# Performance work log

Measured on AMD Instinct MI355X. Metric: run time of the kernel, lower is better.

The kernel has to match this reference:

```python
import jax, jax.numpy as jnp
import numpy as np

K_DEPTH = 3
JAC_A = 1.0  # alpha (Jacobi a)
JAC_B = 1.0  # beta  (Jacobi b)


def jacobi_filter(sig, gammas):
    """Polynomial graph filter g(sigma) = sum_k gamma_k * P_k^{(a,b)}(sigma),
    Jacobi recurrence applied elementwise (Sigma is diagonal spectrum), domain [-1,1],
    fixed inner scalings (fixI=True => alphas=1)."""
    a, b = JAC_A, JAC_B
    xs = [jnp.ones_like(sig)]
    # L = 1
    coef1 = (a - b) / 2.0
    coef2 = (a + b + 2.0) / 2.0
    xs.append(coef1 * xs[0] + coef2 * sig * xs[0])
    for L in range(2, K_DEPTH + 1):
        cl = 2.0 * L * (L + a + b) * (2 * L - 2 + a + b)
        c1 = (2 * L + a + b - 1) * (2 * L + a + b) * (2 * L + a + b - 2)
        c2 = (2 * L + a + b - 1) * (a * a - b * b)
        c3 = 2.0 * (L - 1 + a) * (L - 1 + b) * (2 * L + a + b)
        xs.append((c1 / cl) * sig * xs[-1] - (c2 / cl) * xs[-1] - (c3 / cl) * xs[-2])
    basis = jnp.stack(xs, axis=0)  # [K+1, B, H, L, d]
    return jnp.einsum('k,kbhld->bhld', gammas, basis)


def setup_inputs() -> dict:
    key = jax.random.key(0)
    ks = jax.random.split(key, 7)
    B, L, Ha, Hs, d = 4, 2048, 4, 4, 64
    mk = lambda k, H: jax.random.normal(k, (B, L, H, d), dtype=jnp.float32)
    return {
        'U': mk(ks[0], Ha),
        'Sigma': mk(ks[1], Ha),
        'V': mk(ks[2], Ha),
        'values': mk(ks[3], Ha),
        'queries_softmax': mk(ks[4], Hs),
        'keys_softmax': mk(ks[5], Hs),
        'values_softmax': mk(ks[6], Hs),
        'gammas': jnp.ones((K_DEPTH + 1,), dtype=jnp.float32),
    }


def reference(U, Sigma, V, values, queries_softmax, keys_softmax, values_softmax, gammas):
    d_k = U.shape[-1]
    # ---- AGF (SVD) heads ----
    Uh = jax.nn.softmax(jnp.transpose(U, (0, 2, 1, 3)), axis=-1)        # [B,H,L,d]
    Vt = jax.nn.softmax(jnp.transpose(V, (0, 2, 3, 1)), axis=-1)        # [B,H,d,L]
    vals = jnp.transpose(values, (0, 2, 1, 3))                           # [B,H,L,d]
    sig = jax.nn.sigmoid(jnp.transpose(Sigma, (0, 2, 1, 3)))             # [B,H,L,d]
    gf = jacobi_filter(sig, gammas)                                       # [B,H,L,d]
    kv = jnp.einsum('bhdl,bhle->bhde', Vt, vals)                          # [B,H,d,d]
    out_agf = jnp.einsum('bhld,bhde->bhle', Uh * gf, kv)                  # [B,H,L,d]
    out_agf = jnp.transpose(out_agf, (0, 2, 1, 3))                        # [B,L,H,d]
    # ---- orthogonality loss ----
    eye = jnp.eye(d_k, dtype=Uh.dtype)
    sym_u = jnp.einsum('bhld,bhle->bhde', Uh, Uh) - eye
    sym_v = jnp.einsum('bhdl,bhel->bhde', Vt, Vt) - eye
    ortho_loss = jnp.mean(jnp.abs(sym_u), axis=(1, 2, 3)) + jnp.mean(jnp.abs(sym_v), axis=(1, 2, 3))
    # ---- softmax (flash) heads ----
    q = jnp.transpose(queries_softmax, (0, 2, 1, 3))
    k = jnp.transpose(keys_softmax, (0, 2, 1, 3))
    v = jnp.transpose(values_softmax, (0, 2, 1, 3))
    scores = jnp.einsum('bhld,bhsd->bhls', q, k) / jnp.sqrt(jnp.asarray(d_k, q.dtype))
    attn = jax.nn.softmax(scores, axis=-1)
    out_sm = jnp.einsum('bhls,bhsd->bhld', attn, v)
    out_sm = jnp.transpose(out_sm, (0, 2, 1, 3))                          # [B,L,H,d]
    out = jnp.concatenate([out_agf, out_sm], axis=2)                      # [B,L,2H,d]
    return out, ortho_loss
```

## Files before the change

kernel.cpp:

```cpp
#include <hip/hip_runtime.h>
#include <hip/hip_bf16.h>

#define BB 4
#define SEQ 2048
#define NH 4
#define D 64
#define NPAIR 16
#define HOUT 8
#define LOSS_BASE ((size_t)BB * SEQ * HOUT * D)

#define OFF_PART 0
#define N_PART   (8 * 16 * 3 * 4096)
#define OFF_SPART (OFF_PART + N_PART)
#define N_SPART  (16 * 32 * 64)
#define OFF_LPART (OFF_SPART + N_SPART)
#define N_LPART  (2 * 16 * 4 * 2048)
#define OFF_OPART (OFF_LPART + N_LPART)
#define N_OPART  (2 * 16 * 2048 * 64)
#define OFF_US   (OFF_OPART + N_OPART)
#define USZ ((size_t)16 * 2048 * 64)

typedef __attribute__((ext_vector_type(8))) short bf16x8;
typedef __attribute__((ext_vector_type(4))) float f32x4;
typedef __attribute__((ext_vector_type(8))) unsigned short us8;
typedef __attribute__((ext_vector_type(4))) unsigned short us4;

__device__ __forceinline__ unsigned short f2bf(float x) {
    union { float f; unsigned u; } v; v.f = x;
    unsigned r = v.u + 0x7fffu + ((v.u >> 16) & 1u);
    return (unsigned short)(r >> 16);
}
__device__ __forceinline__ float bf2f(unsigned short u) {
    union { unsigned u; float f; } v; v.u = ((unsigned)u) << 16; return v.f;
}
__device__ __forceinline__ void load16(const float* p, float* v) {
    const float4* q = (const float4*)p;
    float4 a = q[0], b = q[1], c = q[2], d = q[3];
    v[0]=a.x; v[1]=a.y; v[2]=a.z; v[3]=a.w;
    v[4]=b.x; v[5]=b.y; v[6]=b.z; v[7]=b.w;
    v[8]=c.x; v[9]=c.y; v[10]=c.z; v[11]=c.w;
    v[12]=d.x; v[13]=d.y; v[14]=d.z; v[15]=d.w;
}
__device__ __forceinline__ void wr_bf16x16(unsigned short* dst, const float* v) {
    us8 w0, w1;
#pragma unroll
    for (int i = 0; i < 8; i++) { w0[i] = f2bf(v[i]); w1[i] = f2bf(v[8 + i]); }
    *(us8*)dst = w0; *(us8*)(dst + 8) = w1;
}

__global__ __launch_bounds__(256) void prep(const float* __restrict__ U, const float* __restrict__ Vagf,
                                            const float* __restrict__ vals, const float* __restrict__ Ksm,
                                            const float* __restrict__ Vsm,
                                            float* __restrict__ ws, unsigned short* __restrict__ usb,
                                            float* __restrict__ out) {
    int lt = blockIdx.x, p = blockIdx.y;
    int b = p >> 2, h = p & 3;
    int tid = threadIdx.x;
    int r = tid >> 2;
    int c4 = tid & 3;
    int c0 = c4 * 16;
    __shared__ float T[64][68];
    unsigned short* Khi   = usb;
    unsigned short* VbfT  = usb + USZ;
    unsigned short* UhT   = usb + 2 * USZ;
    unsigned short* EhiT  = usb + 3 * USZ;
    unsigned short* EloT  = usb + 4 * USZ;
    unsigned short* valsT = usb + 5 * USZ;
    float* Spart = ws + OFF_SPART;

    const size_t gbase = ((size_t)(b * SEQ + lt * 64 + r) * NH + h) * D + c0;
    const size_t tbase = ((size_t)p * 64 + r) * 2048 + lt * 64 + c0;
    float v[16], e[16];

    load16(U + gbase, v);
    float mx = v[0];
#pragma unroll
    for (int k = 1; k < 16; k++) mx = fmaxf(mx, v[k]);
    mx = fmaxf(mx, __shfl_xor(mx, 1));
    mx = fmaxf(mx, __shfl_xor(mx, 2));
    float sm = 0.0f;
#pragma unroll
    for (int k = 0; k < 16; k++) { v[k] = __expf(v[k] - mx); sm += v[k]; }
    sm += __shfl_xor(sm, 1);
    sm += __shfl_xor(sm, 2);
    float inv = 1.0f / sm;
#pragma unroll
    for (int k = 0; k < 16; k++) T[r][c0 + k] = v[k] * inv;
    __syncthreads();
#pragma unroll
    for (int k = 0; k < 16; k++) e[k] = T[c0 + k][r];
    wr_bf16x16(UhT + tbase, e);
    __syncthreads();

    load16(Vagf + gbase, v);
#pragma unroll
    for (int k = 0; k < 16; k++) T[r][c0 + k] = __expf(v[k]);
    __syncthreads();
    float ssum = 0.0f;
#pragma unroll
    for (int k = 0; k < 16; k++) { e[k] = T[c0 + k][r]; ssum += e[k]; }
    ssum += __shfl_xor(ssum, 1);
    ssum += __shfl_xor(ssum, 2);
    if (c4 == 0) Spart[(p * 32 + lt) * 64 + r] = ssum;
    {
        us8 h0, h1, l0, l1;
#pragma unroll
        for (int i = 0; i < 8; i++) {
            unsigned short hh = f2bf(e[i]);
            h0[i] = hh; l0[i] = f2bf(e[i] - bf2f(hh));
            unsigned short h2 = f2bf(e[8 + i]);
            h1[i] = h2; l1[i] = f2bf(e[8 + i] - bf2f(h2));
        }
        *(us8*)(EhiT + tbase) = h0; *(us8*)(EhiT + tbase + 8) = h1;
        *(us8*)(EloT + tbase) = l0; *(us8*)(EloT + tbase + 8) = l1;
    }
    __syncthreads();

    load16(vals + gbase, v);
#pragma unroll
    for (int k = 0; k < 16; k++) T[r][c0 + k] = v[k];
    __syncthreads();
#pragma unroll
    for (int k = 0; k < 16; k++) e[k] = T[c0 + k][r];
    wr_bf16x16(valsT + tbase, e);
    __syncthreads();

    load16(Vsm + gbase, v);
#pragma unroll
    for (int k = 0; k < 16; k++) T[r][c0 + k] = v[k];
    __syncthreads();
#pragma unroll
    for (int k = 0; k < 16; k++) e[k] = T[c0 + k][r];
    wr_bf16x16(VbfT + tbase, e);

    load16(Ksm + gbase, v);
    wr_bf16x16(Khi + ((size_t)(p * SEQ + lt * 64 + r)) * 64 + c0, v);

    if (lt == 0 && p == 0 && tid < BB) out[LOSS_BASE + tid] = 0.0f;
}

#define PSTR 72
#define FIXM 10.0f

__global__ __launch_bounds__(256, 3) void mid(const unsigned short* __restrict__ usb,
                                              const float* __restrict__ Q,
                                              float* __restrict__ part,
                                              float* __restrict__ Opart, float* __restrict__ lpart) {
    __shared__ __align__(16) unsigned char smem[20480];
    const int bid = blockIdx.x;
    const int tid = threadIdx.x;
    const int w = tid >> 6, lane = tid & 63, lm = lane & 15, quad = lane >> 4;

    if (bid < 1024) {
        int qt = bid & 31, p = (bid >> 5) & 15, half = bid >> 9;
        int b = p >> 2, h = p & 3;
        const unsigned short* Khi  = usb;
        const unsigned short* VbfT = usb + USZ;
        unsigned short* Ph = (unsigned short*)smem;

        bf16x8 qhi[4][2], qlo[4][2];
#pragma unroll
        for (int nq = 0; nq < 4; nq++) {
            const float* qp = Q + ((size_t)(b * SEQ + qt * 64 + nq * 16 + lm) * NH + h) * D + quad * 8;
#pragma unroll
            for (int ks = 0; ks < 2; ks++) {
                float4 a0 = *(const float4*)(qp + ks * 32);
                float4 a1 = *(const float4*)(qp + ks * 32 + 4);
                float qq[8] = {a0.x, a0.y, a0.z, a0.w, a1.x, a1.y, a1.z, a1.w};
#pragma unroll
                for (int j = 0; j < 8; j++) {
                    float xs = qq[j] * 0.125f;
                    unsigned short hi = f2bf(xs);
                    qhi[nq][ks][j] = (short)hi;
                    qlo[nq][ks][j] = (short)f2bf(xs - bf2f(hi));
                }
            }
        }

        float rsum[4] = {0.f, 0.f, 0.f, 0.f};
        f32x4 o[4];
#pragma unroll
        for (int t = 0; t < 4; t++) o[t] = (f32x4){0.f, 0.f, 0.f, 0.f};

        const size_t kbase = ((size_t)p * SEQ + (size_t)half * 1024 + w * 16 + lm) * 64 + quad * 8;
        const size_t vbase = ((size_t)p * 64 + w * 16 + lm) * 2048 + (size_t)half * 1024 + quad * 8;
        bf16x8 kf[2], vf[2], kf2[2], vf2[2];
#pragma unroll
        for (int ks = 0; ks < 2; ks++) {
            kf[ks] = *(const bf16x8*)(Khi + kbase + ks * 32);
            vf[ks] = *(const bf16x8*)(VbfT + vbase + ks * 32);
        }

        for (int it = 0; it < 16; ++it) {
            f32x4 s[4];
#pragma unroll
            for (int t = 0; t < 4; t++) s[t] = (f32x4){0.f, 0.f, 0.f, 0.f};
#pragma unroll
            for (int ks = 0; ks < 2; ks++)
#pragma unroll
                for (int nq = 0; nq < 4; nq++) {
                    s[nq] = __builtin_amdgcn_mfma_f32_16x16x32_bf16(kf[ks], qhi[nq][ks], s[nq], 0, 0, 0);
                    s[nq] = __builtin_amdgcn_mfma_f32_16x16x32_bf16(kf[ks], qlo[nq][ks], s[nq], 0, 0, 0);
                }
            if (it < 15) {
#pragma unroll
                for (int ks = 0; ks < 2; ks++) {
                    kf2[ks] = *(const bf16x8*)(Khi + kbase + (it + 1) * 64ull * 64 + ks * 32);
                    vf2[ks] = *(const bf16x8*)(VbfT + vbase + (it + 1) * 64 + ks * 32);
                }
            }
#pragma unroll
            for (int nq = 0; nq < 4; nq++) {
                us4 pk;
#pragma unroll
                for (int r = 0; r < 4; r++) {
                    float e = __expf(s[nq][r] - FIXM);
                    rsum[nq] += e;
                    pk[r] = f2bf(e);
                }
                *(us4*)&Ph[(nq * 16 + lm) * PSTR + w * 16 + quad * 4] = pk;
            }
            __syncthreads();

#pragma unroll
            for (int ks = 0; ks < 2; ks++)
#pragma unroll
                for (int nq = 0; nq < 4; nq++) {
                    bf16x8 pf = *(const bf16x8*)&Ph[(nq * 16 + lm) * PSTR + ks * 32 + quad * 8];
                    o[nq] = __builtin_amdgcn_mfma_f32_16x16x32_bf16(vf[ks], pf, o[nq], 0, 0, 0);
                }
            __syncthreads();
#pragma unroll
            for (int ks = 0; ks < 2; ks++) { kf[ks] = kf2[ks]; vf[ks] = vf2[ks]; }
        }

#pragma unroll
        for (int nq = 0; nq < 4; nq++) {
            float rs = rsum[nq];
            rs += __shfl_xor(rs, 16);
            rs += __shfl_xor(rs, 32);
            int row = qt * 64 + nq * 16 + lm;
            *(f32x4*)(Opart + ((size_t)(half * 16 + p) * SEQ + row) * 64 + w * 16 + quad * 4) = o[nq];
            if (quad == 0)
                lpart[((size_t)(half * 16 + p) * 4 + w) * SEQ + row] = rs;
        }
    } else {
        int j = bid - 1024;
        int split = j >> 4, p = j & 15;
        const unsigned short* UhT   = usb + 2 * USZ;
        const unsigned short* EhiT  = usb + 3 * USZ;
        const unsigned short* EloT  = usb + 4 * USZ;
        const unsigned short* valsT = usb + 5 * USZ;
        unsigned short* Ut = (unsigned short*)smem;
        unsigned short* Eh = Ut + 64 * 40;
        unsigned short* El = Eh + 64 * 40;
        unsigned short* Vt = El + 64 * 40;
        f32x4 su[4], sv[4], kv[4];
#pragma unroll
        for (int i = 0; i < 4; i++) { su[i] = (f32x4){0,0,0,0}; sv[i] = (f32x4){0,0,0,0}; kv[i] = (f32x4){0,0,0,0}; }
        int srow = tid >> 2;
        int sseg = (tid & 3) * 8;

        for (int step = 0; step < 8; ++step) {
            int l0 = split * 256 + step * 32;
            __syncthreads();
            size_t gb = ((size_t)p * 64 + srow) * 2048 + l0 + sseg;
            *(us8*)&Ut[srow * 40 + sseg] = *(const us8*)(UhT + gb);
            *(us8*)&Eh[srow * 40 + sseg] = *(const us8*)(EhiT + gb);
            *(us8*)&El[srow * 40 + sseg] = *(const us8*)(EloT + gb);
            *(us8*)&Vt[srow * 40 + sseg] = *(const us8*)(valsT + gb);
            __syncthreads();
            int ao = (w * 16 + lm) * 40 + quad * 8;
            bf16x8 au  = *(const bf16x8*)&Ut[ao];
            bf16x8 aeh = *(const bf16x8*)&Eh[ao];
            bf16x8 ael = *(const bf16x8*)&El[ao];
#pragma unroll
            for (int nt = 0; nt < 4; nt++) {
                int bo = (nt * 16 + lm) * 40 + quad * 8;
                bf16x8 bu  = *(const bf16x8*)&Ut[bo];
                bf16x8 beh = *(const bf16x8*)&Eh[bo];
                bf16x8 bv  = *(const bf16x8*)&Vt[bo];
                su[nt] = __builtin_amdgcn_mfma_f32_16x16x32_bf16(au,  bu,  su[nt], 0, 0, 0);
                sv[nt] = __builtin_amdgcn_mfma_f32_16x16x32_bf16(aeh, beh, sv[nt], 0, 0, 0);
                kv[nt] = __builtin_amdgcn_mfma_f32_16x16x32_bf16(aeh, bv,  kv[nt], 0, 0, 0);
                kv[nt] = __builtin_amdgcn_mfma_f32_16x16x32_bf16(ael, bv,  kv[nt], 0, 0, 0);
            }
        }
        float* dst = part + (size_t)(split * 16 + p) * 3 * 4096;
#pragma unroll
        for (int nt = 0; nt < 4; nt++)
#pragma unroll
            for (int reg = 0; reg < 4; reg++) {
                int off = (w * 16 + quad * 4 + reg) * 64 + nt * 16 + lm;
                dst[off] = su[nt][reg];
                dst[4096 + off] = sv[nt][reg];
                dst[8192 + off] = kv[nt][reg];
            }
    }
}

__global__ __launch_bounds__(256) void post(const float* __restrict__ U, const float* __restrict__ Sg,
                                            const float* __restrict__ gam, const float* __restrict__ part,
                                            const float* __restrict__ Spart, const float* __restrict__ Opart,
                                            const float* __restrict__ lpart, float* __restrict__ out) {
    const int bid = blockIdx.x;
    const int tid = threadIdx.x;
    if (bid < 2048) {
        int idx = bid * 256 + tid;
        int p = idx >> 15;
        int rem = idx & 32767;
        int l = rem >> 4, dq = rem & 15;
        int b = p >> 2, h = p & 3;
        f32x4 a = *(const f32x4*)(Opart + ((size_t)p * SEQ + l) * 64 + dq * 4);
        f32x4 c = *(const f32x4*)(Opart + ((size_t)(16 + p) * SEQ + l) * 64 + dq * 4);
        float den = 0.0f;
#pragma unroll
        for (int hf = 0; hf < 2; hf++)
#pragma unroll
            for (int wv = 0; wv < 4; wv++)
                den += lpart[((size_t)(hf * 16 + p) * 4 + wv) * SEQ + l];
        *(f32x4*)(out + ((size_t)(b * SEQ + l) * HOUT + 4 + h) * D + dq * 4) = (a + c) * (1.0f / den);
        return;
    }
    int j = bid - 2048;
    int p = j / 33, lt = j % 33;
    __shared__ float cis[64];
    __shared__ float red[4][64];
    {
        int d = tid & 63, grp = tid >> 6;
        float s = 0.0f;
#pragma unroll
        for (int i = 0; i < 8; i++) s += Spart[(p * 32 + grp * 8 + i) * 64 + d];
        red[grp][d] = s;
        __syncthreads();
        if (tid < 64) cis[tid] = 1.0f / (red[0][tid] + red[1][tid] + red[2][tid] + red[3][tid]);
        __syncthreads();
    }
    if (lt == 32) {
        float s = 0.0f;
        for (int idx = tid; idx < 8192; idx += 256) {
            int g = idx >> 12, i = idx & 4095;
            float v = 0.0f;
#pragma unroll
            for (int sp = 0; sp < 8; sp++) v += part[((size_t)(sp * 16 + p) * 3 + g) * 4096 + i];
            if (g) v *= cis[i >> 6] * cis[i & 63];
            float dg = ((i >> 6) == (i & 63)) ? 1.0f : 0.0f;
            s += fabsf(v - dg);
        }
#pragma unroll
        for (int o = 32; o > 0; o >>= 1) s += __shfl_xor(s, o);
        __shared__ float r4[4];
        if ((tid & 63) == 0) r4[tid >> 6] = s;
        __syncthreads();
        if (tid == 0) atomicAdd(&out[LOSS_BASE + (p >> 2)], (r4[0] + r4[1] + r4[2] + r4[3]) * (1.0f / 16384.0f));
        return;
    }
    int b = p >> 2, h = p & 3;
    __shared__ __align__(16) float kvs[64][68];
    __shared__ __align__(16) float ugs[64][68];
    for (int idx = tid; idx < 4096; idx += 256) {
        float v = 0.0f;
#pragma unroll
        for (int sp = 0; sp < 8; sp++) v += part[((size_t)(sp * 16 + p) * 3 + 2) * 4096 + idx];
        kvs[idx >> 6][idx & 63] = v * cis[idx >> 6];
    }
    {
        int row = tid >> 2;
        int c16 = (tid & 3) * 16;
        size_t ibase = ((size_t)((b * SEQ + lt * 64 + row) * NH + h)) * D + c16;
        float uv[16];
        load16(U + ibase, uv);
        float mx = uv[0];
#pragma unroll
        for (int k = 1; k < 16; k++) mx = fmaxf(mx, uv[k]);
        mx = fmaxf(mx, __shfl_xor(mx, 1));
        mx = fmaxf(mx, __shfl_xor(mx, 2));
        float sm = 0.0f;
#pragma unroll
        for (int k = 0; k < 16; k++) { uv[k] = __expf(uv[k] - mx); sm += uv[k]; }
        sm += __shfl_xor(sm, 1);
        sm += __shfl_xor(sm, 2);
        float inv = 1.0f / sm;
        float sg[16];
        load16(Sg + ibase, sg);
        float g0 = gam[0], g1 = gam[1], g2 = gam[2], g3 = gam[3];
#pragma unroll
        for (int k = 0; k < 16; k++) {
            float sig = 1.0f / (1.0f + __expf(-sg[k]));
            float x1 = 2.0f * sig;
            float x2 = 1.875f * sig * x1 - 0.75f;
            float x3 = 1.8666666666666667f * sig * x2 - 0.8f * x1;
            float gf = g0 + g1 * x1 + g2 * x2 + g3 * x3;
            ugs[row][c16 + k] = uv[k] * inv * gf;
        }
    }
    __syncthreads();
    int tx = tid & 15, ty = tid >> 4;
    float acc[4][4] = {};
#pragma unroll 8
    for (int x = 0; x < 64; x++) {
        float4 kt = *(const float4*)&kvs[x][tx * 4];
        float kb[4] = {kt.x, kt.y, kt.z, kt.w};
#pragma unroll
        for (int a = 0; a < 4; a++) {
            float ua = ugs[ty * 4 + a][x];
#pragma unroll
            for (int e2 = 0; e2 < 4; e2++) acc[a][e2] = fmaf(ua, kb[e2], acc[a][e2]);
        }
    }
#pragma unroll
    for (int a = 0; a < 4; a++)
#pragma unroll
        for (int e2 = 0; e2 < 4; e2++)
            out[((size_t)(b * SEQ + lt * 64 + ty * 4 + a) * HOUT + h) * D + tx * 4 + e2] = acc[a][e2];
}

extern "C" void kernel_launch(void* const* d_in, const int* in_sizes, int n_in,
                              void* d_out, int out_size, void* d_ws, size_t ws_size,
                              hipStream_t stream) {
    (void)in_sizes; (void)n_in; (void)out_size; (void)ws_size;
    const float* U    = (const float*)d_in[0];
    const float* Sg   = (const float*)d_in[1];
    const float* V    = (const float*)d_in[2];
    const float* vals = (const float*)d_in[3];
    const float* Qs   = (const float*)d_in[4];
    const float* Ks   = (const float*)d_in[5];
    const float* Vv   = (const float*)d_in[6];
    const float* gam  = (const float*)d_in[7];
    float* out = (float*)d_out;

    float* ws = (float*)d_ws;
    float* part  = ws + OFF_PART;
    float* Spart = ws + OFF_SPART;
    float* lpart = ws + OFF_LPART;
    float* Opart = ws + OFF_OPART;
    unsigned short* usb = (unsigned short*)(ws + OFF_US);

    prep<<<dim3(32, 16), 256, 0, stream>>>(U, V, vals, Ks, Vv, ws, usb, out);
    mid<<<1152, 256, 0, stream>>>(usb, Qs, part, Opart, lpart);
    post<<<2576, 256, 0, stream>>>(U, Sg, gam, part, Spart, Opart, lpart, out);
}
```

Baseline: 180.7 us.

## Restructure softmax attention to per-wave full KV sweep and MFMA AGF output

The softmax-attention blocks stop splitting the key range into two halves. Each wave now owns 16 query rows and sweeps all keys, with register double-buffered K/V loads and no block-wide barriers. It normalizes and writes the output directly, which removes the Opart/lpart partial buffers and their combine pass in post. The fixed exp offset is also dropped, so exp(s) runs unshifted. The AGF filter product U*gf is moved into prep and stored as bf16 hi/lo, and post computes (U*gf)@kv with split-bf16 MFMA instead of scalar FMA loops. The costs are fewer, longer-running attention blocks at lower occupancy (launch bounds 2), extra workspace traffic for the hi/lo U*gf tensors, and possible overflow risk from dropping the exp shift.

```diff
diff --git a/kernel.cpp b/kernel.cpp
--- a/kernel.cpp
+++ b/kernel.cpp
@@ -13,11 +13,7 @@
 #define N_PART   (8 * 16 * 3 * 4096)
 #define OFF_SPART (OFF_PART + N_PART)
 #define N_SPART  (16 * 32 * 64)
-#define OFF_LPART (OFF_SPART + N_SPART)
-#define N_LPART  (2 * 16 * 4 * 2048)
-#define OFF_OPART (OFF_LPART + N_LPART)
-#define N_OPART  (2 * 16 * 2048 * 64)
-#define OFF_US   (OFF_OPART + N_OPART)
+#define OFF_US   (OFF_SPART + N_SPART)
 #define USZ ((size_t)16 * 2048 * 64)
 
 typedef __attribute__((ext_vector_type(8))) short bf16x8;
@@ -48,17 +44,17 @@
     *(us8*)dst = w0; *(us8*)(dst + 8) = w1;
 }
 
-__global__ __launch_bounds__(256) void prep(const float* __restrict__ U, const float* __restrict__ Vagf,
-                                            const float* __restrict__ vals, const float* __restrict__ Ksm,
-                                            const float* __restrict__ Vsm,
+__global__ __launch_bounds__(256) void prep(const float* __restrict__ U, const float* __restrict__ Sg,
+                                            const float* __restrict__ Vagf, const float* __restrict__ vals,
+                                            const float* __restrict__ Ksm, const float* __restrict__ Vsm,
+                                            const float* __restrict__ gam,
                                             float* __restrict__ ws, unsigned short* __restrict__ usb,
                                             float* __restrict__ out) {
     int lt = blockIdx.x, p = blockIdx.y;
     int b = p >> 2, h = p & 3;
     int tid = threadIdx.x;
     int r = tid >> 2;
-    int c4 = tid & 3;
-    int c0 = c4 * 16;
+    int c0 = (tid & 3) * 16;
     __shared__ float T[64][68];
     unsigned short* Khi   = usb;
     unsigned short* VbfT  = usb + USZ;
@@ -66,9 +62,12 @@
     unsigned short* EhiT  = usb + 3 * USZ;
     unsigned short* EloT  = usb + 4 * USZ;
     unsigned short* valsT = usb + 5 * USZ;
+    unsigned short* Ughi  = usb + 6 * USZ;
+    unsigned short* Uglo  = usb + 7 * USZ;
     float* Spart = ws + OFF_SPART;
 
     const size_t gbase = ((size_t)(b * SEQ + lt * 64 + r) * NH + h) * D + c0;
+    const size_t nbase = ((size_t)(p * SEQ + lt * 64 + r)) * 64 + c0;
     const size_t tbase = ((size_t)p * 64 + r) * 2048 + lt * 64 + c0;
     float v[16], e[16];
 
@@ -85,7 +84,26 @@
     sm += __shfl_xor(sm, 2);
     float inv = 1.0f / sm;
 #pragma unroll
-    for (int k = 0; k < 16; k++) T[r][c0 + k] = v[k] * inv;
+    for (int k = 0; k < 16; k++) { v[k] *= inv; T[r][c0 + k] = v[k]; }
+    {
+        float sg[16];
+        load16(Sg + gbase, sg);
+        float g0 = gam[0], g1 = gam[1], g2 = gam[2], g3 = gam[3];
+        us8 h0, h1, l0, l1;
+#pragma unroll
+        for (int k = 0; k < 16; k++) {
+            float sig = 1.0f / (1.0f + __expf(-sg[k]));
+            float x1 = 2.0f * sig;
+            float x2 = 1.875f * sig * x1 - 0.75f;
+            float x3 = 1.8666666666666667f * sig * x2 - 0.8f * x1;
+            float ug = v[k] * (g0 + g1 * x1 + g2 * x2 + g3 * x3);
+            unsigned short hh = f2bf(ug);
+            unsigned short ll = f2bf(ug - bf2f(hh));
+            if (k < 8) { h0[k] = hh; l0[k] = ll; } else { h1[k - 8] = hh; l1[k - 8] = ll; }
+        }
+        *(us8*)(Ughi + nbase) = h0; *(us8*)(Ughi + nbase + 8) = h1;
+        *(us8*)(Uglo + nbase) = l0; *(us8*)(Uglo + nbase + 8) = l1;
+    }
     __syncthreads();
 #pragma unroll
     for (int k = 0; k < 16; k++) e[k] = T[c0 + k][r];
@@ -101,7 +119,7 @@
     for (int k = 0; k < 16; k++) { e[k] = T[c0 + k][r]; ssum += e[k]; }
     ssum += __shfl_xor(ssum, 1);
     ssum += __shfl_xor(ssum, 2);
-    if (c4 == 0) Spart[(p * 32 + lt) * 64 + r] = ssum;
+    if ((tid & 3) == 0) Spart[(p * 32 + lt) * 64 + r] = ssum;
     {
         us8 h0, h1, l0, l1;
 #pragma unroll
@@ -134,119 +152,121 @@
     wr_bf16x16(VbfT + tbase, e);
 
     load16(Ksm + gbase, v);
-    wr_bf16x16(Khi + ((size_t)(p * SEQ + lt * 64 + r)) * 64 + c0, v);
+    wr_bf16x16(Khi + nbase, v);
 
     if (lt == 0 && p == 0 && tid < BB) out[LOSS_BASE + tid] = 0.0f;
 }
 
 #define PSTR 72
-#define FIXM 10.0f
-
-__global__ __launch_bounds__(256, 3) void mid(const unsigned short* __restrict__ usb,
+
+__global__ __launch_bounds__(256, 2) void mid(const unsigned short* __restrict__ usb,
                                               const float* __restrict__ Q,
-                                              float* __restrict__ part,
-                                              float* __restrict__ Opart, float* __restrict__ lpart) {
+                                              float* __restrict__ part, float* __restrict__ out) {
     __shared__ __align__(16) unsigned char smem[20480];
     const int bid = blockIdx.x;
     const int tid = threadIdx.x;
     const int w = tid >> 6, lane = tid & 63, lm = lane & 15, quad = lane >> 4;
 
-    if (bid < 1024) {
-        int qt = bid & 31, p = (bid >> 5) & 15, half = bid >> 9;
+    if (bid >= 128) {
+        int fb = bid - 128;
+        int qt = fb & 31, p = fb >> 5;
         int b = p >> 2, h = p & 3;
         const unsigned short* Khi  = usb;
         const unsigned short* VbfT = usb + USZ;
-        unsigned short* Ph = (unsigned short*)smem;
-
-        bf16x8 qhi[4][2], qlo[4][2];
-#pragma unroll
-        for (int nq = 0; nq < 4; nq++) {
-            const float* qp = Q + ((size_t)(b * SEQ + qt * 64 + nq * 16 + lm) * NH + h) * D + quad * 8;
+        unsigned short* Ph = (unsigned short*)smem + (size_t)w * 16 * PSTR;
+
+        const int qrow = qt * 64 + w * 16 + lm;
+        bf16x8 qhi[2], qlo[2];
+        {
+            const float* qp = Q + ((size_t)(b * SEQ + qrow) * NH + h) * D + quad * 8;
 #pragma unroll
             for (int ks = 0; ks < 2; ks++) {
+                float qq[8];
                 float4 a0 = *(const float4*)(qp + ks * 32);
                 float4 a1 = *(const float4*)(qp + ks * 32 + 4);
-                float qq[8] = {a0.x, a0.y, a0.z, a0.w, a1.x, a1.y, a1.z, a1.w};
+                qq[0]=a0.x; qq[1]=a0.y; qq[2]=a0.z; qq[3]=a0.w;
+                qq[4]=a1.x; qq[5]=a1.y; qq[6]=a1.z; qq[7]=a1.w;
 #pragma unroll
                 for (int j = 0; j < 8; j++) {
                     float xs = qq[j] * 0.125f;
                     unsigned short hi = f2bf(xs);
-                    qhi[nq][ks][j] = (short)hi;
-                    qlo[nq][ks][j] = (short)f2bf(xs - bf2f(hi));
+                    qhi[ks][j] = (short)hi;
+                    qlo[ks][j] = (short)f2bf(xs - bf2f(hi));
                 }
             }
         }
 
-        float rsum[4] = {0.f, 0.f, 0.f, 0.f};
+        float rsum = 0.0f;
         f32x4 o[4];
 #pragma unroll
         for (int t = 0; t < 4; t++) o[t] = (f32x4){0.f, 0.f, 0.f, 0.f};
 
-        const size_t kbase = ((size_t)p * SEQ + (size_t)half * 1024 + w * 16 + lm) * 64 + quad * 8;
-        const size_t vbase = ((size_t)p * 64 + w * 16 + lm) * 2048 + (size_t)half * 1024 + quad * 8;
-        bf16x8 kf[2], vf[2], kf2[2], vf2[2];
-#pragma unroll
-        for (int ks = 0; ks < 2; ks++) {
-            kf[ks] = *(const bf16x8*)(Khi + kbase + ks * 32);
-            vf[ks] = *(const bf16x8*)(VbfT + vbase + ks * 32);
-        }
-
-        for (int it = 0; it < 16; ++it) {
+        const size_t kbase = ((size_t)p * SEQ + lm) * 64 + quad * 8;
+        const size_t vbase = ((size_t)p * 64 + lm) * 2048 + quad * 8;
+
+        bf16x8 kc[4][2], vc[4][2], kn[4][2], vn[4][2];
+#pragma unroll
+        for (int t = 0; t < 4; t++)
+#pragma unroll
+            for (int ks = 0; ks < 2; ks++) {
+                kc[t][ks] = *(const bf16x8*)(Khi + kbase + (size_t)(t * 16) * 64 + ks * 32);
+                vc[t][ks] = *(const bf16x8*)(VbfT + vbase + (size_t)(t * 16) * 2048 + ks * 32);
+            }
+
+        for (int kt = 0; kt < 32; ++kt) {
+            if (kt < 31) {
+#pragma unroll
+                for (int t = 0; t < 4; t++)
+#pragma unroll
+                    for (int ks = 0; ks < 2; ks++) {
+                        kn[t][ks] = *(const bf16x8*)(Khi + kbase + (size_t)((kt + 1) * 64 + t * 16) * 64 + ks * 32);
+                        vn[t][ks] = *(const bf16x8*)(VbfT + vbase + (size_t)(t * 16) * 2048 + (kt + 1) * 64 + ks * 32);
+                    }
+            }
             f32x4 s[4];
 #pragma unroll
             for (int t = 0; t < 4; t++) s[t] = (f32x4){0.f, 0.f, 0.f, 0.f};
 #pragma unroll
-            for (int ks = 0; ks < 2; ks++)
-#pragma unroll
-                for (int nq = 0; nq < 4; nq++) {
-                    s[nq] = __builtin_amdgcn_mfma_f32_16x16x32_bf16(kf[ks], qhi[nq][ks], s[nq], 0, 0, 0);
-                    s[nq] = __builtin_amdgcn_mfma_f32_16x16x32_bf16(kf[ks], qlo[nq][ks], s[nq], 0, 0, 0);
+            for (int t = 0; t < 4; t++)
+#pragma unroll
+                for (int ks = 0; ks < 2; ks++) {
+                    s[t] = __builtin_amdgcn_mfma_f32_16x16x32_bf16(kc[t][ks], qhi[ks], s[t], 0, 0, 0);
+                    s[t] = __builtin_amdgcn_mfma_f32_16x16x32_bf16(kc[t][ks], qlo[ks], s[t], 0, 0, 0);
                 }
-            if (it < 15) {
-#pragma unroll
-                for (int ks = 0; ks < 2; ks++) {
-                    kf2[ks] = *(const bf16x8*)(Khi + kbase + (it + 1) * 64ull * 64 + ks * 32);
-                    vf2[ks] = *(const bf16x8*)(VbfT + vbase + (it + 1) * 64 + ks * 32);
-                }
-            }
-#pragma unroll
-            for (int nq = 0; nq < 4; nq++) {
-                us4 pk;
-#pragma unroll
-                for (int r = 0; r < 4; r++) {
-                    float e = __expf(s[nq][r] - FIXM);
-                    rsum[nq] += e;
-                    pk[r] = f2bf(e);
-                }
-                *(us4*)&Ph[(nq * 16 + lm) * PSTR + w * 16 + quad * 4] = pk;
-            }
-            __syncthreads();
-
-#pragma unroll
-            for (int ks = 0; ks < 2; ks++)
-#pragma unroll
-                for (int nq = 0; nq < 4; nq++) {
-                    bf16x8 pf = *(const bf16x8*)&Ph[(nq * 16 + lm) * PSTR + ks * 32 + quad * 8];
-                    o[nq] = __builtin_amdgcn_mfma_f32_16x16x32_bf16(vf[ks], pf, o[nq], 0, 0, 0);
-                }
-            __syncthreads();
-#pragma unroll
-            for (int ks = 0; ks < 2; ks++) { kf[ks] = kf2[ks]; vf[ks] = vf2[ks]; }
-        }
-
-#pragma unroll
-        for (int nq = 0; nq < 4; nq++) {
-            float rs = rsum[nq];
-            rs += __shfl_xor(rs, 16);
-            rs += __shfl_xor(rs, 32);
-            int row = qt * 64 + nq * 16 + lm;
-            *(f32x4*)(Opart + ((size_t)(half * 16 + p) * SEQ + row) * 64 + w * 16 + quad * 4) = o[nq];
-            if (quad == 0)
-                lpart[((size_t)(half * 16 + p) * 4 + w) * SEQ + row] = rs;
-        }
+#pragma unroll
+            for (int t = 0; t < 4; t++) {
+                float e0 = __expf(s[t][0]);
+                float e1 = __expf(s[t][1]);
+                float e2 = __expf(s[t][2]);
+                float e3 = __expf(s[t][3]);
+                rsum += (e0 + e1) + (e2 + e3);
+                union { __hip_bfloat162 h2[2]; us4 u4; } pk;
+                pk.h2[0] = __float22bfloat162_rn(make_float2(e0, e1));
+                pk.h2[1] = __float22bfloat162_rn(make_float2(e2, e3));
+                *(us4*)&Ph[lm * PSTR + t * 16 + quad * 4] = pk.u4;
+            }
+            bf16x8 pf0 = *(const bf16x8*)&Ph[lm * PSTR + quad * 8];
+            bf16x8 pf1 = *(const bf16x8*)&Ph[lm * PSTR + 32 + quad * 8];
+#pragma unroll
+            for (int dt = 0; dt < 4; dt++) {
+                o[dt] = __builtin_amdgcn_mfma_f32_16x16x32_bf16(vc[dt][0], pf0, o[dt], 0, 0, 0);
+                o[dt] = __builtin_amdgcn_mfma_f32_16x16x32_bf16(vc[dt][1], pf1, o[dt], 0, 0, 0);
+            }
+#pragma unroll
+            for (int t = 0; t < 4; t++)
+#pragma unroll
+                for (int ks = 0; ks < 2; ks++) { kc[t][ks] = kn[t][ks]; vc[t][ks] = vn[t][ks]; }
+        }
+
+        rsum += __shfl_xor(rsum, 16);
+        rsum += __shfl_xor(rsum, 32);
+        float invd = 1.0f / rsum;
+        float* op = out + ((size_t)(b * SEQ + qrow) * HOUT + 4 + h) * D + quad * 4;
+#pragma unroll
+        for (int dt = 0; dt < 4; dt++)
+            *(f32x4*)(op + dt * 16) = o[dt] * invd;
     } else {
-        int j = bid - 1024;
-        int split = j >> 4, p = j & 15;
+        int split = bid >> 4, p = bid & 15;
         const unsigned short* UhT   = usb + 2 * USZ;
         const unsigned short* EhiT  = usb + 3 * USZ;
         const unsigned short* EloT  = usb + 4 * USZ;
@@ -299,33 +319,16 @@
     }
 }
 
-__global__ __launch_bounds__(256) void post(const float* __restrict__ U, const float* __restrict__ Sg,
-                                            const float* __restrict__ gam, const float* __restrict__ part,
-                                            const float* __restrict__ Spart, const float* __restrict__ Opart,
-                                            const float* __restrict__ lpart, float* __restrict__ out) {
+__global__ __launch_bounds__(256) void post(const float* __restrict__ part, const float* __restrict__ Spart,
+                                            const unsigned short* __restrict__ usb, float* __restrict__ out) {
     const int bid = blockIdx.x;
     const int tid = threadIdx.x;
-    if (bid < 2048) {
-        int idx = bid * 256 + tid;
-        int p = idx >> 15;
-        int rem = idx & 32767;
-        int l = rem >> 4, dq = rem & 15;
-        int b = p >> 2, h = p & 3;
-        f32x4 a = *(const f32x4*)(Opart + ((size_t)p * SEQ + l) * 64 + dq * 4);
-        f32x4 c = *(const f32x4*)(Opart + ((size_t)(16 + p) * SEQ + l) * 64 + dq * 4);
-        float den = 0.0f;
-#pragma unroll
-        for (int hf = 0; hf < 2; hf++)
-#pragma unroll
-            for (int wv = 0; wv < 4; wv++)
-                den += lpart[((size_t)(hf * 16 + p) * 4 + wv) * SEQ + l];
-        *(f32x4*)(out + ((size_t)(b * SEQ + l) * HOUT + 4 + h) * D + dq * 4) = (a + c) * (1.0f / den);
-        return;
-    }
-    int j = bid - 2048;
-    int p = j / 33, lt = j % 33;
+    const int w = tid >> 6, lane = tid & 63, lm = lane & 15, quad = lane >> 4;
+    int p = (bid < 512) ? (bid >> 5) : (bid - 512);
     __shared__ float cis[64];
     __shared__ float red[4][64];
+    __shared__ __align__(16) unsigned short KVh[64 * PSTR];
+    __shared__ __align__(16) unsigned short KVl[64 * PSTR];
     {
         int d = tid & 63, grp = tid >> 6;
         float s = 0.0f;
@@ -336,7 +339,7 @@
         if (tid < 64) cis[tid] = 1.0f / (red[0][tid] + red[1][tid] + red[2][tid] + red[3][tid]);
         __syncthreads();
     }
-    if (lt == 32) {
+    if (bid >= 512) {
         float s = 0.0f;
         for (int idx = tid; idx < 8192; idx += 256) {
             int g = idx >> 12, i = idx & 4095;
@@ -349,70 +352,54 @@
         }
 #pragma unroll
         for (int o = 32; o > 0; o >>= 1) s += __shfl_xor(s, o);
-        __shared__ float r4[4];
-        if ((tid & 63) == 0) r4[tid >> 6] = s;
+        if ((tid & 63) == 0) red[0][(tid >> 6) * 2] = s;
         __syncthreads();
-        if (tid == 0) atomicAdd(&out[LOSS_BASE + (p >> 2)], (r4[0] + r4[1] + r4[2] + r4[3]) * (1.0f / 16384.0f));
+        if (tid == 0)
+            atomicAdd(&out[LOSS_BASE + (p >> 2)],
+                      (red[0][0] + red[0][2] + red[0][4] + red[0][6]) * (1.0f / 16384.0f));
         return;
     }
+    int lt = bid & 31;
     int b = p >> 2, h = p & 3;
-    __shared__ __align__(16) float kvs[64][68];
-    __shared__ __align__(16) float ugs[64][68];
+    const unsigned short* Ughi = usb + 6 * USZ;
+    const unsigned short* Uglo = usb + 7 * USZ;
     for (int idx = tid; idx < 4096; idx += 256) {
+        int d = idx >> 6, e = idx & 63;
         float v = 0.0f;
 #pragma unroll
         for (int sp = 0; sp < 8; sp++) v += part[((size_t)(sp * 16 + p) * 3 + 2) * 4096 + idx];
-        kvs[idx >> 6][idx & 63] = v * cis[idx >> 6];
-    }
-    {
-        int row = tid >> 2;
-        int c16 = (tid & 3) * 16;
-        size_t ibase = ((size_t)((b * SEQ + lt * 64 + row) * NH + h)) * D + c16;
-        float uv[16];
-        load16(U + ibase, uv);
-        float mx = uv[0];
-#pragma unroll
-        for (int k = 1; k < 16; k++) mx = fmaxf(mx, uv[k]);
-        mx = fmaxf(mx, __shfl_xor(mx, 1));
-        mx = fmaxf(mx, __shfl_xor(mx, 2));
-        float sm = 0.0f;
-#pragma unroll
-        for (int k = 0; k < 16; k++) { uv[k] = __expf(uv[k] - mx); sm += uv[k]; }
-        sm += __shfl_xor(sm, 1);
-        sm += __shfl_xor(sm, 2);
-        float inv = 1.0f / sm;
-        float sg[16];
-        load16(Sg + ibase, sg);
-        float g0 = gam[0], g1 = gam[1], g2 = gam[2], g3 = gam[3];
-#pragma unroll
-        for (int k = 0; k < 16; k++) {
-            float sig = 1.0f / (1.0f + __expf(-sg[k]));
-            float x1 = 2.0f * sig;
-            float x2 = 1.875f * sig * x1 - 0.75f;
-            float x3 = 1.8666666666666667f * sig * x2 - 0.8f * x1;
-            float gf = g0 + g1 * x1 + g2 * x2 + g3 * x3;
-            ugs[row][c16 + k] = uv[k] * inv * gf;
-        }
-    }
-    __syncthreads();
-    int tx = tid & 15, ty = tid >> 4;
-    float acc[4][4] = {};
-#pragma unroll 8
-    for (int x = 0; x < 64; x++) {
-        float4 kt = *(const float4*)&kvs[x][tx * 4];
-        float kb[4] = {kt.x, kt.y, kt.z, kt.w};
-#pragma unroll
-        for (int a = 0; a < 4; a++) {
-            float ua = ugs[ty * 4 + a][x];
-#pragma unroll
-            for (int e2 = 0; e2 < 4; e2++) acc[a][e2] = fmaf(ua, kb[e2], acc[a][e2]);
-        }
-    }
-#pragma unroll
-    for (int a = 0; a < 4; a++)
-#pragma unroll
-        for (int e2 = 0; e2 < 4; e2++)
-            out[((size_t)(b * SEQ + lt * 64 + ty * 4 + a) * HOUT + h) * D + tx * 4 + e2] = acc[a][e2];
+        v *= cis[d];
+        unsigned short hh = f2bf(v);
+        KVh[e * PSTR + d] = hh;
+        KVl[e * PSTR + d] = f2bf(v - bf2f(hh));
+    }
+    __syncthreads();
+    size_t ub = ((size_t)(p * SEQ + lt * 64 + w * 16 + lm)) * 64 + quad * 8;
+    bf16x8 ah[2], al[2];
+#pragma unroll
+    for (int ks = 0; ks < 2; ks++) {
+        ah[ks] = *(const bf16x8*)(Ughi + ub + ks * 32);
+        al[ks] = *(const bf16x8*)(Uglo + ub + ks * 32);
+    }
+    f32x4 acc[4];
+#pragma unroll
+    for (int nt = 0; nt < 4; nt++) acc[nt] = (f32x4){0.f, 0.f, 0.f, 0.f};
+#pragma unroll
+    for (int nt = 0; nt < 4; nt++)
+#pragma unroll
+        for (int ks = 0; ks < 2; ks++) {
+            bf16x8 bh = *(const bf16x8*)&KVh[(nt * 16 + lm) * PSTR + ks * 32 + quad * 8];
+            bf16x8 bl = *(const bf16x8*)&KVl[(nt * 16 + lm) * PSTR + ks * 32 + quad * 8];
+            acc[nt] = __builtin_amdgcn_mfma_f32_16x16x32_bf16(ah[ks], bh, acc[nt], 0, 0, 0);
+            acc[nt] = __builtin_amdgcn_mfma_f32_16x16x32_bf16(al[ks], bh, acc[nt], 0, 0, 0);
+            acc[nt] = __builtin_amdgcn_mfma_f32_16x16x32_bf16(ah[ks], bl, acc[nt], 0, 0, 0);
+        }
+#pragma unroll
+    for (int nt = 0; nt < 4; nt++)
+#pragma unroll
+        for (int reg = 0; reg < 4; reg++)
+            out[((size_t)(b * SEQ + lt * 64 + w * 16 + quad * 4 + reg) * HOUT + h) * D + nt * 16 + lm] =
+                acc[nt][reg];
 }
 
 extern "C" void kernel_launch(void* const* d_in, const int* in_sizes, int n_in,
@@ -432,11 +419,9 @@
     float* ws = (float*)d_ws;
     float* part  = ws + OFF_PART;
     float* Spart = ws + OFF_SPART;
-    float* lpart = ws + OFF_LPART;
-    float* Opart = ws + OFF_OPART;
     unsigned short* usb = (unsigned short*)(ws + OFF_US);
 
-    prep<<<dim3(32, 16), 256, 0, stream>>>(U, V, vals, Ks, Vv, ws, usb, out);
-    mid<<<1152, 256, 0, stream>>>(usb, Qs, part, Opart, lpart);
-    post<<<2576, 256, 0, stream>>>(U, Sg, gam, part, Spart, Opart, lpart, out);
-}
+    prep<<<dim3(32, 16), 256, 0, stream>>>(U, Sg, V, vals, Ks, Vv, gam, ws, usb, out);
+    mid<<<640, 256, 0, stream>>>(usb, Qs, part, out);
+    post<<<528, 256, 0, stream>>>(part, Spart, usb, out);
+}
```

Measured after the change: 247.5 us. 1.37x slower.
